# Optimization experiments

Hardware: AMD Instinct MI355X
Metric: run time of the kernel (lower is better)

The kernel has to match this reference:

```python
import jax, jax.numpy as jnp
import numpy as np

N = 10000   # function nodes
E = 160000  # edges (avg in/out degree ~16)
C = 8       # hidden channels per function node (fix_hidden_channels=True)
B = 64      # batch
EPS = 1e-5


def setup_inputs() -> dict:
    key = jax.random.key(0)
    ks = jax.random.split(key, 6)
    x = jax.random.normal(ks[0], (B, E), jnp.float32)
    # xavier-ish scale for fan_in ~ avg_degree=16
    w1 = jax.random.normal(ks[1], (E, C), jnp.float32) * 0.25
    b1 = jnp.zeros((N, C), jnp.float32)
    w3 = jax.random.normal(ks[2], (E, C), jnp.float32) * 0.25
    b3 = jnp.zeros((E,), jnp.float32)
    gamma = jnp.ones((N, C), jnp.float32)
    beta = jnp.zeros((N, C), jnp.float32)
    edge_src = jax.random.randint(ks[3], (E,), 0, N, dtype=jnp.int32)
    edge_dst = jax.random.randint(ks[4], (E,), 0, N, dtype=jnp.int32)
    return dict(x=x, w1=w1, b1=b1, gamma=gamma, beta=beta, w3=w3, b3=b3,
                edge_src=edge_src, edge_dst=edge_dst)


def reference(x, w1, b1, gamma, beta, w3, b3, edge_src, edge_dst):
    # --- lin1: SparseLinear (E -> N*C); W1[e, (v,k)] != 0 iff v == dst(e) ---
    # out1[b, v, k] = sum_{e: dst(e)==v} x[b, e] * w1[e, k] + b1[v, k]
    vals = x.T[:, :, None] * w1[:, None, :]                    # [E, B, C]
    h = jax.ops.segment_sum(vals, edge_dst, num_segments=N)    # [N, B, C]
    h = jnp.transpose(h, (1, 0, 2)) + b1                       # [B, N, C]
    # --- GroupLayerNorm: normalize over each node's C-channel group ---
    mu = jnp.mean(h, axis=-1, keepdims=True)
    var = jnp.var(h, axis=-1, keepdims=True)
    h = (h - mu) * jax.lax.rsqrt(var + EPS) * gamma + beta
    # --- nonlin (ELU); dropout p=0 in eval mode -> identity ---
    h = jax.nn.elu(h)
    # --- lin3: SparseLinear (N*C -> E); W3[(v,k), e] != 0 iff v == src(e) ---
    # out[b, e] = sum_k h[b, src(e), k] * w3[e, k] + b3[e]
    g = h[:, edge_src, :]                                      # [B, E, C]
    out = jnp.einsum('bec,ec->be', g, w3) + b3                 # [B, E]
    # --- residual ---
    return out + x
```

## Files before the change

### kernel.cpp

```cpp
#include <hip/hip_runtime.h>

#define N_NODES 10000
#define N_EDGES 160000
#define NC 8
#define PAD 64
#define LN_EPS 1e-5f

typedef _Float16 h4_t __attribute__((ext_vector_type(4)));
typedef _Float16 h8_t __attribute__((ext_vector_type(8)));

__device__ __forceinline__ int swz(int e, int b) {
  return e * 64 + ((((b >> 2) ^ ((e >> 2) & 15)) << 2) | (b & 3));
}

__global__ void __launch_bounds__(256) prep_kernel(
    const float* __restrict__ x, const int* __restrict__ edst,
    const float* __restrict__ w1, int* __restrict__ cur_dst,
    _Float16* __restrict__ xT_d, _Float16* __restrict__ w1_h) {
  __shared__ float tile[64 * 64];
  __shared__ int pP[64];
  const int e0 = blockIdx.x * 64;
  const int t = threadIdx.x;

  if (t < 64) {
    const int e = e0 + t;
    const int n = edst[e];
    int r = atomicAdd(&cur_dst[n], 1);
    if (r >= PAD) r = PAD - 1;
    const int p = (n << 6) + r;
    pP[t] = p;
    const float4* wp1 = (const float4*)(w1 + (size_t)e * NC);
    const float4 wa = wp1[0], wb = wp1[1];
    h8_t hw;
    hw[0] = (_Float16)wa.x; hw[1] = (_Float16)wa.y;
    hw[2] = (_Float16)wa.z; hw[3] = (_Float16)wa.w;
    hw[4] = (_Float16)wb.x; hw[5] = (_Float16)wb.y;
    hw[6] = (_Float16)wb.z; hw[7] = (_Float16)wb.w;
    *(h8_t*)&w1_h[(size_t)p * NC] = hw;
  }

  const int u = t & 15;
  const int row = t >> 4;
#pragma unroll
  for (int j = 0; j < 4; ++j) {
    const int b = j * 16 + row;
    const float4 xv = *(const float4*)&x[(size_t)b * N_EDGES + e0 + 4 * u];
    tile[swz(4 * u + 0, b)] = xv.x;
    tile[swz(4 * u + 1, b)] = xv.y;
    tile[swz(4 * u + 2, b)] = xv.z;
    tile[swz(4 * u + 3, b)] = xv.w;
  }
  __syncthreads();
#pragma unroll
  for (int j = 0; j < 4; ++j) {
    const int r = j * 16 + row;
    const float4 vv = *(const float4*)&tile[r * 64 + ((u ^ ((r >> 2) & 15)) << 2)];
    h4_t hv;
    hv[0] = (_Float16)vv.x; hv[1] = (_Float16)vv.y;
    hv[2] = (_Float16)vv.z; hv[3] = (_Float16)vv.w;
    *(h4_t*)&xT_d[(size_t)pP[r] * 64 + 4 * u] = hv;
  }
}

__global__ void __launch_bounds__(256) node_kernel(
    const _Float16* __restrict__ xT_d, const _Float16* __restrict__ w1_h,
    const float* __restrict__ b1, const float* __restrict__ gamma,
    const float* __restrict__ beta, const int* __restrict__ cur_dst,
    _Float16* __restrict__ v) {
  const int n = blockIdx.x * 4 + (threadIdx.x >> 6);
  const int b = threadIdx.x & 63;

  float a[NC];
#pragma unroll
  for (int c = 0; c < NC; ++c) a[c] = 0.f;

  const int s0 = n << 6;
  const int s1 = s0 + cur_dst[n];
  int i = s0;
  for (; i + 4 <= s1; i += 4) {
    float xe[4];
#pragma unroll
    for (int k = 0; k < 4; ++k) xe[k] = (float)xT_d[(size_t)(i + k) * 64 + b];
    h8_t wl[4];
#pragma unroll
    for (int k = 0; k < 4; ++k) wl[k] = *(const h8_t*)&w1_h[(size_t)(i + k) * NC];
#pragma unroll
    for (int k = 0; k < 4; ++k) {
#pragma unroll
      for (int c = 0; c < NC; ++c) a[c] += xe[k] * (float)wl[k][c];
    }
  }
  for (; i < s1; ++i) {
    const float xe = (float)xT_d[(size_t)i * 64 + b];
    const h8_t wl = *(const h8_t*)&w1_h[(size_t)i * NC];
#pragma unroll
    for (int c = 0; c < NC; ++c) a[c] += xe * (float)wl[c];
  }

  const float4* b1p = (const float4*)(b1 + (size_t)n * NC);
  const float4 b1a = b1p[0], b1b = b1p[1];
  a[0] += b1a.x; a[1] += b1a.y; a[2] += b1a.z; a[3] += b1a.w;
  a[4] += b1b.x; a[5] += b1b.y; a[6] += b1b.z; a[7] += b1b.w;

  float mu = 0.f;
#pragma unroll
  for (int c = 0; c < NC; ++c) mu += a[c];
  mu *= 0.125f;
  float var = 0.f;
#pragma unroll
  for (int c = 0; c < NC; ++c) { a[c] -= mu; var += a[c] * a[c]; }
  var *= 0.125f;
  const float rs = rsqrtf(var + LN_EPS);

  const float4* gp = (const float4*)(gamma + (size_t)n * NC);
  const float4 ga = gp[0], gb = gp[1];
  const float4* bp = (const float4*)(beta + (size_t)n * NC);
  const float4 ba = bp[0], bb = bp[1];
  float w[NC];
  w[0] = a[0] * rs * ga.x + ba.x;  w[1] = a[1] * rs * ga.y + ba.y;
  w[2] = a[2] * rs * ga.z + ba.z;  w[3] = a[3] * rs * ga.w + ba.w;
  w[4] = a[4] * rs * gb.x + bb.x;  w[5] = a[5] * rs * gb.y + bb.y;
  w[6] = a[6] * rs * gb.z + bb.z;  w[7] = a[7] * rs * gb.w + bb.w;
#pragma unroll
  for (int c = 0; c < NC; ++c) w[c] = w[c] > 0.f ? w[c] : expm1f(w[c]);

  h8_t hv;
#pragma unroll
  for (int c = 0; c < NC; ++c) hv[c] = (_Float16)w[c];
  *(h8_t*)&v[(size_t)n * 512 + b * NC] = hv;
}

__global__ void __launch_bounds__(256) edge_kernel(
    const _Float16* __restrict__ v, const float* __restrict__ w3,
    const float* __restrict__ b3, const float* __restrict__ x,
    const int* __restrict__ esrc, float* __restrict__ out) {
  __shared__ float tile[64 * 64];
  const int e0 = blockIdx.x * 64;
  const int t = threadIdx.x;
  const int w = t >> 6;
  const int b = t & 63;
  const int u = t & 15;
  const int row = t >> 4;

  int sidx = 0;
  if (b < 16) sidx = esrc[e0 + w * 16 + b];

  h8_t hv[16];
#pragma unroll
  for (int r = 0; r < 16; ++r) {
    const int s = __shfl(sidx, r, 64);
    hv[r] = *(const h8_t*)&v[(size_t)s * 512 + b * NC];
  }
  const float4 bb = *(const float4*)&b3[e0 + 4 * u];
  float4 xb[4];
#pragma unroll
  for (int j = 0; j < 4; ++j) {
    const int bo = j * 16 + row;
    xb[j] = *(const float4*)&x[(size_t)bo * N_EDGES + e0 + 4 * u];
  }

#pragma unroll
  for (int r = 0; r < 16; ++r) {
    const float4* wp = (const float4*)(w3 + (size_t)(e0 + w * 16 + r) * NC);
    const float4 wa = wp[0], wb = wp[1];
    const float dot =
        (float)hv[r][0] * wa.x + (float)hv[r][1] * wa.y +
        (float)hv[r][2] * wa.z + (float)hv[r][3] * wa.w +
        (float)hv[r][4] * wb.x + (float)hv[r][5] * wb.y +
        (float)hv[r][6] * wb.z + (float)hv[r][7] * wb.w;
    tile[swz(w * 16 + r, b)] = dot;
  }
  __syncthreads();

#pragma unroll
  for (int j = 0; j < 4; ++j) {
    const int bo = j * 16 + row;
    const float o0 = tile[swz(4 * u + 0, bo)];
    const float o1 = tile[swz(4 * u + 1, bo)];
    const float o2 = tile[swz(4 * u + 2, bo)];
    const float o3 = tile[swz(4 * u + 3, bo)];
    float4 o;
    o.x = o0 + bb.x + xb[j].x;  o.y = o1 + bb.y + xb[j].y;
    o.z = o2 + bb.z + xb[j].z;  o.w = o3 + bb.w + xb[j].w;
    *(float4*)&out[(size_t)bo * N_EDGES + e0 + 4 * u] = o;
  }
}

extern "C" void kernel_launch(void* const* d_in, const int* in_sizes, int n_in,
                              void* d_out, int out_size, void* d_ws, size_t ws_size,
                              hipStream_t stream) {
  const float* x     = (const float*)d_in[0];
  const float* w1    = (const float*)d_in[1];
  const float* b1    = (const float*)d_in[2];
  const float* gamma = (const float*)d_in[3];
  const float* beta  = (const float*)d_in[4];
  const float* w3    = (const float*)d_in[5];
  const float* b3    = (const float*)d_in[6];
  const int* esrc    = (const int*)d_in[7];
  const int* edst    = (const int*)d_in[8];
  float* out = (float*)d_out;

  char* ws = (char*)d_ws;
  size_t off = 0;
  auto alloc = [&](size_t bytes) -> void* {
    void* p = ws + off;
    off += (bytes + 255) & ~(size_t)255;
    return p;
  };
  _Float16* xT_d = (_Float16*)alloc((size_t)N_NODES * PAD * 64 * 2);
  _Float16* w1_h = (_Float16*)alloc((size_t)N_NODES * PAD * NC * 2);
  _Float16* v    = (_Float16*)alloc((size_t)N_NODES * 512 * 2);
  int* cur_dst   = (int*)alloc((size_t)N_NODES * 4);

  hipMemsetAsync(cur_dst, 0, (size_t)N_NODES * 4, stream);

  prep_kernel<<<N_EDGES / 64, 256, 0, stream>>>(x, edst, w1, cur_dst, xT_d, w1_h);
  node_kernel<<<N_NODES / 4, 256, 0, stream>>>(xT_d, w1_h, b1, gamma, beta,
                                               cur_dst, v);
  edge_kernel<<<N_EDGES / 64, 256, 0, stream>>>(v, w3, b3, x, esrc, out);
}
```

Before: 165.9 us.

## Fuse three kernels and memset into one cooperative persistent kernel with grid syncs

Replaces the memset plus prep, node and edge kernels with a single cooperative kernel. Blocks loop over tiles in grid-stride fashion and are separated by grid.sync barriers, with the grid sized from occupancy. This removes launch gaps between stages, in exchange for grid-wide barrier cost, the loss of __launch_bounds__ (which may raise register pressure), and extra __syncthreads in the looped tiles.

```diff
diff --git a/kernel.cpp b/kernel.cpp
--- a/kernel.cpp
+++ b/kernel.cpp
@@ -1,4 +1,7 @@
 #include <hip/hip_runtime.h>
+#include <hip/hip_cooperative_groups.h>
+
+namespace cg = cooperative_groups;
 
 #define N_NODES 10000
 #define N_EDGES 160000
@@ -13,176 +16,189 @@
   return e * 64 + ((((b >> 2) ^ ((e >> 2) & 15)) << 2) | (b & 3));
 }
 
-__global__ void __launch_bounds__(256) prep_kernel(
-    const float* __restrict__ x, const int* __restrict__ edst,
-    const float* __restrict__ w1, int* __restrict__ cur_dst,
-    _Float16* __restrict__ xT_d, _Float16* __restrict__ w1_h) {
+__global__ void fused_kernel(
+    const float* __restrict__ x, const float* __restrict__ w1,
+    const float* __restrict__ b1, const float* __restrict__ gamma,
+    const float* __restrict__ beta, const float* __restrict__ w3,
+    const float* __restrict__ b3, const int* __restrict__ esrc,
+    const int* __restrict__ edst, float* __restrict__ out,
+    _Float16* __restrict__ xT_d, _Float16* __restrict__ w1_h,
+    _Float16* __restrict__ v, int* __restrict__ cur_dst) {
+  cg::grid_group grid = cg::this_grid();
   __shared__ float tile[64 * 64];
   __shared__ int pP[64];
-  const int e0 = blockIdx.x * 64;
   const int t = threadIdx.x;
-
-  if (t < 64) {
-    const int e = e0 + t;
-    const int n = edst[e];
-    int r = atomicAdd(&cur_dst[n], 1);
-    if (r >= PAD) r = PAD - 1;
-    const int p = (n << 6) + r;
-    pP[t] = p;
-    const float4* wp1 = (const float4*)(w1 + (size_t)e * NC);
-    const float4 wa = wp1[0], wb = wp1[1];
-    h8_t hw;
-    hw[0] = (_Float16)wa.x; hw[1] = (_Float16)wa.y;
-    hw[2] = (_Float16)wa.z; hw[3] = (_Float16)wa.w;
-    hw[4] = (_Float16)wb.x; hw[5] = (_Float16)wb.y;
-    hw[6] = (_Float16)wb.z; hw[7] = (_Float16)wb.w;
-    *(h8_t*)&w1_h[(size_t)p * NC] = hw;
-  }
-
-  const int u = t & 15;
-  const int row = t >> 4;
-#pragma unroll
-  for (int j = 0; j < 4; ++j) {
-    const int b = j * 16 + row;
-    const float4 xv = *(const float4*)&x[(size_t)b * N_EDGES + e0 + 4 * u];
-    tile[swz(4 * u + 0, b)] = xv.x;
-    tile[swz(4 * u + 1, b)] = xv.y;
-    tile[swz(4 * u + 2, b)] = xv.z;
-    tile[swz(4 * u + 3, b)] = xv.w;
-  }
-  __syncthreads();
-#pragma unroll
-  for (int j = 0; j < 4; ++j) {
-    const int r = j * 16 + row;
-    const float4 vv = *(const float4*)&tile[r * 64 + ((u ^ ((r >> 2) & 15)) << 2)];
-    h4_t hv;
-    hv[0] = (_Float16)vv.x; hv[1] = (_Float16)vv.y;
-    hv[2] = (_Float16)vv.z; hv[3] = (_Float16)vv.w;
-    *(h4_t*)&xT_d[(size_t)pP[r] * 64 + 4 * u] = hv;
-  }
-}
-
-__global__ void __launch_bounds__(256) node_kernel(
-    const _Float16* __restrict__ xT_d, const _Float16* __restrict__ w1_h,
-    const float* __restrict__ b1, const float* __restrict__ gamma,
-    const float* __restrict__ beta, const int* __restrict__ cur_dst,
-    _Float16* __restrict__ v) {
-  const int n = blockIdx.x * 4 + (threadIdx.x >> 6);
-  const int b = threadIdx.x & 63;
-
-  float a[NC];
-#pragma unroll
-  for (int c = 0; c < NC; ++c) a[c] = 0.f;
-
-  const int s0 = n << 6;
-  const int s1 = s0 + cur_dst[n];
-  int i = s0;
-  for (; i + 4 <= s1; i += 4) {
-    float xe[4];
-#pragma unroll
-    for (int k = 0; k < 4; ++k) xe[k] = (float)xT_d[(size_t)(i + k) * 64 + b];
-    h8_t wl[4];
-#pragma unroll
-    for (int k = 0; k < 4; ++k) wl[k] = *(const h8_t*)&w1_h[(size_t)(i + k) * NC];
-#pragma unroll
-    for (int k = 0; k < 4; ++k) {
-#pragma unroll
-      for (int c = 0; c < NC; ++c) a[c] += xe[k] * (float)wl[k][c];
+  const int nb = gridDim.x;
+
+  for (int i = blockIdx.x * 256 + t; i < N_NODES; i += nb * 256) cur_dst[i] = 0;
+  grid.sync();
+
+  {
+    const int u = t & 15;
+    const int row = t >> 4;
+    for (int tl = blockIdx.x; tl < N_EDGES / 64; tl += nb) {
+      const int e0 = tl * 64;
+      if (t < 64) {
+        const int e = e0 + t;
+        const int n = edst[e];
+        int r = atomicAdd(&cur_dst[n], 1);
+        if (r >= PAD) r = PAD - 1;
+        const int p = (n << 6) + r;
+        pP[t] = p;
+        const float4* wp1 = (const float4*)(w1 + (size_t)e * NC);
+        const float4 wa = wp1[0], wb = wp1[1];
+        h8_t hw;
+        hw[0] = (_Float16)wa.x; hw[1] = (_Float16)wa.y;
+        hw[2] = (_Float16)wa.z; hw[3] = (_Float16)wa.w;
+        hw[4] = (_Float16)wb.x; hw[5] = (_Float16)wb.y;
+        hw[6] = (_Float16)wb.z; hw[7] = (_Float16)wb.w;
+        *(h8_t*)&w1_h[(size_t)p * NC] = hw;
+      }
+#pragma unroll
+      for (int j = 0; j < 4; ++j) {
+        const int b = j * 16 + row;
+        const float4 xv = *(const float4*)&x[(size_t)b * N_EDGES + e0 + 4 * u];
+        tile[swz(4 * u + 0, b)] = xv.x;
+        tile[swz(4 * u + 1, b)] = xv.y;
+        tile[swz(4 * u + 2, b)] = xv.z;
+        tile[swz(4 * u + 3, b)] = xv.w;
+      }
+      __syncthreads();
+#pragma unroll
+      for (int j = 0; j < 4; ++j) {
+        const int r = j * 16 + row;
+        const float4 vv =
+            *(const float4*)&tile[r * 64 + ((u ^ ((r >> 2) & 15)) << 2)];
+        h4_t hv;
+        hv[0] = (_Float16)vv.x; hv[1] = (_Float16)vv.y;
+        hv[2] = (_Float16)vv.z; hv[3] = (_Float16)vv.w;
+        *(h4_t*)&xT_d[(size_t)pP[r] * 64 + 4 * u] = hv;
+      }
+      __syncthreads();
     }
   }
-  for (; i < s1; ++i) {
-    const float xe = (float)xT_d[(size_t)i * 64 + b];
-    const h8_t wl = *(const h8_t*)&w1_h[(size_t)i * NC];
-#pragma unroll
-    for (int c = 0; c < NC; ++c) a[c] += xe * (float)wl[c];
-  }
-
-  const float4* b1p = (const float4*)(b1 + (size_t)n * NC);
-  const float4 b1a = b1p[0], b1b = b1p[1];
-  a[0] += b1a.x; a[1] += b1a.y; a[2] += b1a.z; a[3] += b1a.w;
-  a[4] += b1b.x; a[5] += b1b.y; a[6] += b1b.z; a[7] += b1b.w;
-
-  float mu = 0.f;
-#pragma unroll
-  for (int c = 0; c < NC; ++c) mu += a[c];
-  mu *= 0.125f;
-  float var = 0.f;
-#pragma unroll
-  for (int c = 0; c < NC; ++c) { a[c] -= mu; var += a[c] * a[c]; }
-  var *= 0.125f;
-  const float rs = rsqrtf(var + LN_EPS);
-
-  const float4* gp = (const float4*)(gamma + (size_t)n * NC);
-  const float4 ga = gp[0], gb = gp[1];
-  const float4* bp = (const float4*)(beta + (size_t)n * NC);
-  const float4 ba = bp[0], bb = bp[1];
-  float w[NC];
-  w[0] = a[0] * rs * ga.x + ba.x;  w[1] = a[1] * rs * ga.y + ba.y;
-  w[2] = a[2] * rs * ga.z + ba.z;  w[3] = a[3] * rs * ga.w + ba.w;
-  w[4] = a[4] * rs * gb.x + bb.x;  w[5] = a[5] * rs * gb.y + bb.y;
-  w[6] = a[6] * rs * gb.z + bb.z;  w[7] = a[7] * rs * gb.w + bb.w;
-#pragma unroll
-  for (int c = 0; c < NC; ++c) w[c] = w[c] > 0.f ? w[c] : expm1f(w[c]);
-
-  h8_t hv;
-#pragma unroll
-  for (int c = 0; c < NC; ++c) hv[c] = (_Float16)w[c];
-  *(h8_t*)&v[(size_t)n * 512 + b * NC] = hv;
-}
-
-__global__ void __launch_bounds__(256) edge_kernel(
-    const _Float16* __restrict__ v, const float* __restrict__ w3,
-    const float* __restrict__ b3, const float* __restrict__ x,
-    const int* __restrict__ esrc, float* __restrict__ out) {
-  __shared__ float tile[64 * 64];
-  const int e0 = blockIdx.x * 64;
-  const int t = threadIdx.x;
-  const int w = t >> 6;
-  const int b = t & 63;
-  const int u = t & 15;
-  const int row = t >> 4;
-
-  int sidx = 0;
-  if (b < 16) sidx = esrc[e0 + w * 16 + b];
-
-  h8_t hv[16];
-#pragma unroll
-  for (int r = 0; r < 16; ++r) {
-    const int s = __shfl(sidx, r, 64);
-    hv[r] = *(const h8_t*)&v[(size_t)s * 512 + b * NC];
-  }
-  const float4 bb = *(const float4*)&b3[e0 + 4 * u];
-  float4 xb[4];
-#pragma unroll
-  for (int j = 0; j < 4; ++j) {
-    const int bo = j * 16 + row;
-    xb[j] = *(const float4*)&x[(size_t)bo * N_EDGES + e0 + 4 * u];
-  }
-
-#pragma unroll
-  for (int r = 0; r < 16; ++r) {
-    const float4* wp = (const float4*)(w3 + (size_t)(e0 + w * 16 + r) * NC);
-    const float4 wa = wp[0], wb = wp[1];
-    const float dot =
-        (float)hv[r][0] * wa.x + (float)hv[r][1] * wa.y +
-        (float)hv[r][2] * wa.z + (float)hv[r][3] * wa.w +
-        (float)hv[r][4] * wb.x + (float)hv[r][5] * wb.y +
-        (float)hv[r][6] * wb.z + (float)hv[r][7] * wb.w;
-    tile[swz(w * 16 + r, b)] = dot;
-  }
-  __syncthreads();
-
-#pragma unroll
-  for (int j = 0; j < 4; ++j) {
-    const int bo = j * 16 + row;
-    const float o0 = tile[swz(4 * u + 0, bo)];
-    const float o1 = tile[swz(4 * u + 1, bo)];
-    const float o2 = tile[swz(4 * u + 2, bo)];
-    const float o3 = tile[swz(4 * u + 3, bo)];
-    float4 o;
-    o.x = o0 + bb.x + xb[j].x;  o.y = o1 + bb.y + xb[j].y;
-    o.z = o2 + bb.z + xb[j].z;  o.w = o3 + bb.w + xb[j].w;
-    *(float4*)&out[(size_t)bo * N_EDGES + e0 + 4 * u] = o;
+  grid.sync();
+
+  {
+    const int wid = t >> 6;
+    const int b = t & 63;
+    for (int g = blockIdx.x; g < N_NODES / 4; g += nb) {
+      const int n = g * 4 + wid;
+
+      float a[NC];
+#pragma unroll
+      for (int c = 0; c < NC; ++c) a[c] = 0.f;
+
+      const int s0 = n << 6;
+      const int s1 = s0 + cur_dst[n];
+      int i = s0;
+      for (; i + 4 <= s1; i += 4) {
+        float xe[4];
+#pragma unroll
+        for (int k = 0; k < 4; ++k) xe[k] = (float)xT_d[(size_t)(i + k) * 64 + b];
+        h8_t wl[4];
+#pragma unroll
+        for (int k = 0; k < 4; ++k) wl[k] = *(const h8_t*)&w1_h[(size_t)(i + k) * NC];
+#pragma unroll
+        for (int k = 0; k < 4; ++k) {
+#pragma unroll
+          for (int c = 0; c < NC; ++c) a[c] += xe[k] * (float)wl[k][c];
+        }
+      }
+      for (; i < s1; ++i) {
+        const float xe = (float)xT_d[(size_t)i * 64 + b];
+        const h8_t wl = *(const h8_t*)&w1_h[(size_t)i * NC];
+#pragma unroll
+        for (int c = 0; c < NC; ++c) a[c] += xe * (float)wl[c];
+      }
+
+      const float4* b1p = (const float4*)(b1 + (size_t)n * NC);
+      const float4 b1a = b1p[0], b1b = b1p[1];
+      a[0] += b1a.x; a[1] += b1a.y; a[2] += b1a.z; a[3] += b1a.w;
+      a[4] += b1b.x; a[5] += b1b.y; a[6] += b1b.z; a[7] += b1b.w;
+
+      float mu = 0.f;
+#pragma unroll
+      for (int c = 0; c < NC; ++c) mu += a[c];
+      mu *= 0.125f;
+      float var = 0.f;
+#pragma unroll
+      for (int c = 0; c < NC; ++c) { a[c] -= mu; var += a[c] * a[c]; }
+      var *= 0.125f;
+      const float rs = rsqrtf(var + LN_EPS);
+
+      const float4* gp = (const float4*)(gamma + (size_t)n * NC);
+      const float4 ga = gp[0], gb = gp[1];
+      const float4* bp = (const float4*)(beta + (size_t)n * NC);
+      const float4 ba = bp[0], bb = bp[1];
+      float w[NC];
+      w[0] = a[0] * rs * ga.x + ba.x;  w[1] = a[1] * rs * ga.y + ba.y;
+      w[2] = a[2] * rs * ga.z + ba.z;  w[3] = a[3] * rs * ga.w + ba.w;
+      w[4] = a[4] * rs * gb.x + bb.x;  w[5] = a[5] * rs * gb.y + bb.y;
+      w[6] = a[6] * rs * gb.z + bb.z;  w[7] = a[7] * rs * gb.w + bb.w;
+#pragma unroll
+      for (int c = 0; c < NC; ++c) w[c] = w[c] > 0.f ? w[c] : expm1f(w[c]);
+
+      h8_t hv;
+#pragma unroll
+      for (int c = 0; c < NC; ++c) hv[c] = (_Float16)w[c];
+      *(h8_t*)&v[(size_t)n * 512 + b * NC] = hv;
+    }
+  }
+  grid.sync();
+
+  {
+    const int w = t >> 6;
+    const int b = t & 63;
+    const int u = t & 15;
+    const int row = t >> 4;
+    for (int tl = blockIdx.x; tl < N_EDGES / 64; tl += nb) {
+      const int e0 = tl * 64;
+
+      int sidx = 0;
+      if (b < 16) sidx = esrc[e0 + w * 16 + b];
+
+      h8_t hv[16];
+#pragma unroll
+      for (int r = 0; r < 16; ++r) {
+        const int s = __shfl(sidx, r, 64);
+        hv[r] = *(const h8_t*)&v[(size_t)s * 512 + b * NC];
+      }
+      const float4 bb = *(const float4*)&b3[e0 + 4 * u];
+      float4 xb[4];
+#pragma unroll
+      for (int j = 0; j < 4; ++j) {
+        const int bo = j * 16 + row;
+        xb[j] = *(const float4*)&x[(size_t)bo * N_EDGES + e0 + 4 * u];
+      }
+
+#pragma unroll
+      for (int r = 0; r < 16; ++r) {
+        const float4* wp = (const float4*)(w3 + (size_t)(e0 + w * 16 + r) * NC);
+        const float4 wa = wp[0], wb = wp[1];
+        const float dot =
+            (float)hv[r][0] * wa.x + (float)hv[r][1] * wa.y +
+            (float)hv[r][2] * wa.z + (float)hv[r][3] * wa.w +
+            (float)hv[r][4] * wb.x + (float)hv[r][5] * wb.y +
+            (float)hv[r][6] * wb.z + (float)hv[r][7] * wb.w;
+        tile[swz(w * 16 + r, b)] = dot;
+      }
+      __syncthreads();
+
+#pragma unroll
+      for (int j = 0; j < 4; ++j) {
+        const int bo = j * 16 + row;
+        const float o0 = tile[swz(4 * u + 0, bo)];
+        const float o1 = tile[swz(4 * u + 1, bo)];
+        const float o2 = tile[swz(4 * u + 2, bo)];
+        const float o3 = tile[swz(4 * u + 3, bo)];
+        float4 o;
+        o.x = o0 + bb.x + xb[j].x;  o.y = o1 + bb.y + xb[j].y;
+        o.z = o2 + bb.z + xb[j].z;  o.w = o3 + bb.w + xb[j].w;
+        *(float4*)&out[(size_t)bo * N_EDGES + e0 + 4 * u] = o;
+      }
+      __syncthreads();
+    }
   }
 }
 
@@ -212,10 +228,20 @@
   _Float16* v    = (_Float16*)alloc((size_t)N_NODES * 512 * 2);
   int* cur_dst   = (int*)alloc((size_t)N_NODES * 4);
 
-  hipMemsetAsync(cur_dst, 0, (size_t)N_NODES * 4, stream);
-
-  prep_kernel<<<N_EDGES / 64, 256, 0, stream>>>(x, edst, w1, cur_dst, xT_d, w1_h);
-  node_kernel<<<N_NODES / 4, 256, 0, stream>>>(xT_d, w1_h, b1, gamma, beta,
-                                               cur_dst, v);
-  edge_kernel<<<N_EDGES / 64, 256, 0, stream>>>(v, w3, b3, x, esrc, out);
+  static int grid_blocks = 0;
+  if (grid_blocks == 0) {
+    int bpc = 0;
+    if (hipOccupancyMaxActiveBlocksPerMultiprocessor(&bpc, fused_kernel, 256, 0)
+            != hipSuccess || bpc < 1)
+      bpc = 2;
+    grid_blocks = bpc * 256;
+    if (grid_blocks > 2500) grid_blocks = 2500;
+  }
+
+  void* kargs[] = {(void*)&x,    (void*)&w1,   (void*)&b1,  (void*)&gamma,
+                   (void*)&beta, (void*)&w3,   (void*)&b3,  (void*)&esrc,
+                   (void*)&edst, (void*)&out,  (void*)&xT_d, (void*)&w1_h,
+                   (void*)&v,    (void*)&cur_dst};
+  hipLaunchCooperativeKernel((const void*)fused_kernel, dim3(grid_blocks),
+                             dim3(256), kargs, 0, stream);
 }
```

After: 402.7 us. 2.43x slower.

## Store edge index lists instead of scattering transposed x and w1 by destination

Applied to the files above, without the earlier changes.

The prep kernel no longer scatters the transposed x rows and the fp16 w1 rows into per-destination padded slots. It writes x transposed in edge order plus a per-node list of edge ids, and the node kernel gathers through that list, reading w1 directly in fp32. This turns the scattered writes in prep into coalesced ones and shrinks the padded workspace. In exchange the node kernel does an extra dependent index load and random gathers, with w1 now read at full precision. Overflow beyond PAD edges per node now drops those edges, where before they overwrote the last slot.

```diff
diff --git a/kernel.cpp b/kernel.cpp
--- a/kernel.cpp
+++ b/kernel.cpp
@@ -13,30 +13,19 @@
   return e * 64 + ((((b >> 2) ^ ((e >> 2) & 15)) << 2) | (b & 3));
 }
 
-__global__ void __launch_bounds__(256) prep_kernel(
+__global__ void __launch_bounds__(256) transpose_kernel(
     const float* __restrict__ x, const int* __restrict__ edst,
-    const float* __restrict__ w1, int* __restrict__ cur_dst,
-    _Float16* __restrict__ xT_d, _Float16* __restrict__ w1_h) {
+    int* __restrict__ cur_dst, _Float16* __restrict__ xT,
+    int* __restrict__ ein) {
   __shared__ float tile[64 * 64];
-  __shared__ int pP[64];
   const int e0 = blockIdx.x * 64;
   const int t = threadIdx.x;
 
   if (t < 64) {
     const int e = e0 + t;
     const int n = edst[e];
-    int r = atomicAdd(&cur_dst[n], 1);
-    if (r >= PAD) r = PAD - 1;
-    const int p = (n << 6) + r;
-    pP[t] = p;
-    const float4* wp1 = (const float4*)(w1 + (size_t)e * NC);
-    const float4 wa = wp1[0], wb = wp1[1];
-    h8_t hw;
-    hw[0] = (_Float16)wa.x; hw[1] = (_Float16)wa.y;
-    hw[2] = (_Float16)wa.z; hw[3] = (_Float16)wa.w;
-    hw[4] = (_Float16)wb.x; hw[5] = (_Float16)wb.y;
-    hw[6] = (_Float16)wb.z; hw[7] = (_Float16)wb.w;
-    *(h8_t*)&w1_h[(size_t)p * NC] = hw;
+    const int r = atomicAdd(&cur_dst[n], 1);
+    if (r < PAD) ein[(n << 6) + r] = e;
   }
 
   const int u = t & 15;
@@ -58,15 +47,15 @@
     h4_t hv;
     hv[0] = (_Float16)vv.x; hv[1] = (_Float16)vv.y;
     hv[2] = (_Float16)vv.z; hv[3] = (_Float16)vv.w;
-    *(h4_t*)&xT_d[(size_t)pP[r] * 64 + 4 * u] = hv;
+    *(h4_t*)&xT[(size_t)(e0 + r) * 64 + 4 * u] = hv;
   }
 }
 
 __global__ void __launch_bounds__(256) node_kernel(
-    const _Float16* __restrict__ xT_d, const _Float16* __restrict__ w1_h,
-    const float* __restrict__ b1, const float* __restrict__ gamma,
-    const float* __restrict__ beta, const int* __restrict__ cur_dst,
-    _Float16* __restrict__ v) {
+    const _Float16* __restrict__ xT, const int* __restrict__ ein,
+    const float* __restrict__ w1, const float* __restrict__ b1,
+    const float* __restrict__ gamma, const float* __restrict__ beta,
+    const int* __restrict__ cur_dst, _Float16* __restrict__ v) {
   const int n = blockIdx.x * 4 + (threadIdx.x >> 6);
   const int b = threadIdx.x & 63;
 
@@ -75,26 +64,39 @@
   for (int c = 0; c < NC; ++c) a[c] = 0.f;
 
   const int s0 = n << 6;
-  const int s1 = s0 + cur_dst[n];
+  const int deg = min(cur_dst[n], PAD);
+  const int s1 = s0 + deg;
   int i = s0;
   for (; i + 4 <= s1; i += 4) {
+    int e[4];
+#pragma unroll
+    for (int k = 0; k < 4; ++k) e[k] = ein[i + k];
     float xe[4];
 #pragma unroll
-    for (int k = 0; k < 4; ++k) xe[k] = (float)xT_d[(size_t)(i + k) * 64 + b];
-    h8_t wl[4];
-#pragma unroll
-    for (int k = 0; k < 4; ++k) wl[k] = *(const h8_t*)&w1_h[(size_t)(i + k) * NC];
+    for (int k = 0; k < 4; ++k) xe[k] = (float)xT[(size_t)e[k] * 64 + b];
+    float4 wa[4], wb[4];
 #pragma unroll
     for (int k = 0; k < 4; ++k) {
-#pragma unroll
-      for (int c = 0; c < NC; ++c) a[c] += xe[k] * (float)wl[k][c];
+      const float4* wp = (const float4*)(w1 + (size_t)e[k] * NC);
+      wa[k] = wp[0]; wb[k] = wp[1];
     }
+#pragma unroll
+    for (int k = 0; k < 4; ++k) {
+      a[0] += xe[k] * wa[k].x;  a[1] += xe[k] * wa[k].y;
+      a[2] += xe[k] * wa[k].z;  a[3] += xe[k] * wa[k].w;
+      a[4] += xe[k] * wb[k].x;  a[5] += xe[k] * wb[k].y;
+      a[6] += xe[k] * wb[k].z;  a[7] += xe[k] * wb[k].w;
+    }
   }
   for (; i < s1; ++i) {
-    const float xe = (float)xT_d[(size_t)i * 64 + b];
-    const h8_t wl = *(const h8_t*)&w1_h[(size_t)i * NC];
-#pragma unroll
-    for (int c = 0; c < NC; ++c) a[c] += xe * (float)wl[c];
+    const int e = ein[i];
+    const float xe = (float)xT[(size_t)e * 64 + b];
+    const float4* wp = (const float4*)(w1 + (size_t)e * NC);
+    const float4 wa = wp[0], wb = wp[1];
+    a[0] += xe * wa.x;  a[1] += xe * wa.y;
+    a[2] += xe * wa.z;  a[3] += xe * wa.w;
+    a[4] += xe * wb.x;  a[5] += xe * wb.y;
+    a[6] += xe * wb.z;  a[7] += xe * wb.w;
   }
 
   const float4* b1p = (const float4*)(b1 + (size_t)n * NC);
@@ -207,15 +209,15 @@
     off += (bytes + 255) & ~(size_t)255;
     return p;
   };
-  _Float16* xT_d = (_Float16*)alloc((size_t)N_NODES * PAD * 64 * 2);
-  _Float16* w1_h = (_Float16*)alloc((size_t)N_NODES * PAD * NC * 2);
-  _Float16* v    = (_Float16*)alloc((size_t)N_NODES * 512 * 2);
-  int* cur_dst   = (int*)alloc((size_t)N_NODES * 4);
+  _Float16* xT  = (_Float16*)alloc((size_t)N_EDGES * 64 * 2);
+  int* ein      = (int*)alloc((size_t)N_NODES * PAD * 4);
+  _Float16* v   = (_Float16*)alloc((size_t)N_NODES * 512 * 2);
+  int* cur_dst  = (int*)alloc((size_t)N_NODES * 4);
 
   hipMemsetAsync(cur_dst, 0, (size_t)N_NODES * 4, stream);
 
-  prep_kernel<<<N_EDGES / 64, 256, 0, stream>>>(x, edst, w1, cur_dst, xT_d, w1_h);
-  node_kernel<<<N_NODES / 4, 256, 0, stream>>>(xT_d, w1_h, b1, gamma, beta,
+  transpose_kernel<<<N_EDGES / 64, 256, 0, stream>>>(x, edst, cur_dst, xT, ein);
+  node_kernel<<<N_NODES / 4, 256, 0, stream>>>(xT, ein, w1, b1, gamma, beta,
                                                cur_dst, v);
   edge_kernel<<<N_EDGES / 64, 256, 0, stream>>>(v, w3, b3, x, esrc, out);
 }
```

After: 169.3 us. 2.1% more time.

## Process 256 edges per block in prep and edge kernels

Applied to the files above, without the earlier changes.

Both the prep and edge kernels now handle 256 edges per block instead of 64. The prep kernel stages x in a padded fp16 shared tile, so the transpose and precision conversion happen together. The edge kernel loops over four 64-edge sub-tiles, holds all outputs in registers and writes them at the end. This cuts block count to 625, meant to lower per-block overhead and give wider contiguous row segments. The cost is more registers per thread and fewer blocks to spread across CUs, which may hurt latency hiding.

```diff
diff --git a/kernel.cpp b/kernel.cpp
--- a/kernel.cpp
+++ b/kernel.cpp
@@ -17,12 +17,12 @@
     const float* __restrict__ x, const int* __restrict__ edst,
     const float* __restrict__ w1, int* __restrict__ cur_dst,
     _Float16* __restrict__ xT_d, _Float16* __restrict__ w1_h) {
-  __shared__ float tile[64 * 64];
-  __shared__ int pP[64];
-  const int e0 = blockIdx.x * 64;
+  __shared__ _Float16 tile[256 * 72];
+  __shared__ int pP[256];
+  const int e0 = blockIdx.x * 256;
   const int t = threadIdx.x;
 
-  if (t < 64) {
+  {
     const int e = e0 + t;
     const int n = edst[e];
     int r = atomicAdd(&cur_dst[n], 1);
@@ -42,23 +42,25 @@
   const int u = t & 15;
   const int row = t >> 4;
 #pragma unroll
-  for (int j = 0; j < 4; ++j) {
-    const int b = j * 16 + row;
-    const float4 xv = *(const float4*)&x[(size_t)b * N_EDGES + e0 + 4 * u];
-    tile[swz(4 * u + 0, b)] = xv.x;
-    tile[swz(4 * u + 1, b)] = xv.y;
-    tile[swz(4 * u + 2, b)] = xv.z;
-    tile[swz(4 * u + 3, b)] = xv.w;
+  for (int s = 0; s < 4; ++s) {
+#pragma unroll
+    for (int j = 0; j < 4; ++j) {
+      const int b = j * 16 + row;
+      const float4 xv =
+          *(const float4*)&x[(size_t)b * N_EDGES + e0 + 64 * s + 4 * u];
+      const int el = 64 * s + 4 * u;
+      tile[(el + 0) * 72 + b] = (_Float16)xv.x;
+      tile[(el + 1) * 72 + b] = (_Float16)xv.y;
+      tile[(el + 2) * 72 + b] = (_Float16)xv.z;
+      tile[(el + 3) * 72 + b] = (_Float16)xv.w;
+    }
   }
   __syncthreads();
 #pragma unroll
-  for (int j = 0; j < 4; ++j) {
-    const int r = j * 16 + row;
-    const float4 vv = *(const float4*)&tile[r * 64 + ((u ^ ((r >> 2) & 15)) << 2)];
-    h4_t hv;
-    hv[0] = (_Float16)vv.x; hv[1] = (_Float16)vv.y;
-    hv[2] = (_Float16)vv.z; hv[3] = (_Float16)vv.w;
-    *(h4_t*)&xT_d[(size_t)pP[r] * 64 + 4 * u] = hv;
+  for (int m = 0; m < 16; ++m) {
+    const int rr = m * 16 + row;
+    const h4_t hv = *(const h4_t*)&tile[rr * 72 + 4 * u];
+    *(h4_t*)&xT_d[(size_t)pP[rr] * 64 + 4 * u] = hv;
   }
 }
 
@@ -135,54 +137,68 @@
     const float* __restrict__ b3, const float* __restrict__ x,
     const int* __restrict__ esrc, float* __restrict__ out) {
   __shared__ float tile[64 * 64];
-  const int e0 = blockIdx.x * 64;
+  const int e0 = blockIdx.x * 256;
   const int t = threadIdx.x;
   const int w = t >> 6;
   const int b = t & 63;
   const int u = t & 15;
   const int row = t >> 4;
 
-  int sidx = 0;
-  if (b < 16) sidx = esrc[e0 + w * 16 + b];
-
-  h8_t hv[16];
-#pragma unroll
-  for (int r = 0; r < 16; ++r) {
-    const int s = __shfl(sidx, r, 64);
-    hv[r] = *(const h8_t*)&v[(size_t)s * 512 + b * NC];
-  }
-  const float4 bb = *(const float4*)&b3[e0 + 4 * u];
-  float4 xb[4];
+  float4 bb[4];
+#pragma unroll
+  for (int p = 0; p < 4; ++p)
+    bb[p] = *(const float4*)&b3[e0 + p * 64 + 4 * u];
+
+  float4 ob[4][4];
+#pragma unroll
+  for (int p = 0; p < 4; ++p) {
+    const int ep = e0 + p * 64;
+    int sidx = 0;
+    if (b < 16) sidx = esrc[ep + w * 16 + b];
+
+    h8_t hv[16];
+#pragma unroll
+    for (int r = 0; r < 16; ++r) {
+      const int s = __shfl(sidx, r, 64);
+      hv[r] = *(const h8_t*)&v[(size_t)s * 512 + b * NC];
+    }
+
+#pragma unroll
+    for (int r = 0; r < 16; ++r) {
+      const float4* wp = (const float4*)(w3 + (size_t)(ep + w * 16 + r) * NC);
+      const float4 wa = wp[0], wb = wp[1];
+      const float dot =
+          (float)hv[r][0] * wa.x + (float)hv[r][1] * wa.y +
+          (float)hv[r][2] * wa.z + (float)hv[r][3] * wa.w +
+          (float)hv[r][4] * wb.x + (float)hv[r][5] * wb.y +
+          (float)hv[r][6] * wb.z + (float)hv[r][7] * wb.w;
+      tile[swz(w * 16 + r, b)] = dot;
+    }
+    __syncthreads();
+
+#pragma unroll
+    for (int j = 0; j < 4; ++j) {
+      const int bo = j * 16 + row;
+      const float o0 = tile[swz(4 * u + 0, bo)];
+      const float o1 = tile[swz(4 * u + 1, bo)];
+      const float o2 = tile[swz(4 * u + 2, bo)];
+      const float o3 = tile[swz(4 * u + 3, bo)];
+      const float4 xb = *(const float4*)&x[(size_t)bo * N_EDGES + ep + 4 * u];
+      float4 o;
+      o.x = o0 + bb[p].x + xb.x;  o.y = o1 + bb[p].y + xb.y;
+      o.z = o2 + bb[p].z + xb.z;  o.w = o3 + bb[p].w + xb.w;
+      ob[p][j] = o;
+    }
+    __syncthreads();
+  }
+
 #pragma unroll
   for (int j = 0; j < 4; ++j) {
     const int bo = j * 16 + row;
-    xb[j] = *(const float4*)&x[(size_t)bo * N_EDGES + e0 + 4 * u];
-  }
-
-#pragma unroll
-  for (int r = 0; r < 16; ++r) {
-    const float4* wp = (const float4*)(w3 + (size_t)(e0 + w * 16 + r) * NC);
-    const float4 wa = wp[0], wb = wp[1];
-    const float dot =
-        (float)hv[r][0] * wa.x + (float)hv[r][1] * wa.y +
-        (float)hv[r][2] * wa.z + (float)hv[r][3] * wa.w +
-        (float)hv[r][4] * wb.x + (float)hv[r][5] * wb.y +
-        (float)hv[r][6] * wb.z + (float)hv[r][7] * wb.w;
-    tile[swz(w * 16 + r, b)] = dot;
-  }
-  __syncthreads();
-
-#pragma unroll
-  for (int j = 0; j < 4; ++j) {
-    const int bo = j * 16 + row;
-    const float o0 = tile[swz(4 * u + 0, bo)];
-    const float o1 = tile[swz(4 * u + 1, bo)];
-    const float o2 = tile[swz(4 * u + 2, bo)];
-    const float o3 = tile[swz(4 * u + 3, bo)];
-    float4 o;
-    o.x = o0 + bb.x + xb[j].x;  o.y = o1 + bb.y + xb[j].y;
-    o.z = o2 + bb.z + xb[j].z;  o.w = o3 + bb.w + xb[j].w;
-    *(float4*)&out[(size_t)bo * N_EDGES + e0 + 4 * u] = o;
+#pragma unroll
+    for (int p = 0; p < 4; ++p) {
+      *(float4*)&out[(size_t)bo * N_EDGES + e0 + p * 64 + 4 * u] = ob[p][j];
+    }
   }
 }
 
@@ -214,8 +230,8 @@
 
   hipMemsetAsync(cur_dst, 0, (size_t)N_NODES * 4, stream);
 
-  prep_kernel<<<N_EDGES / 64, 256, 0, stream>>>(x, edst, w1, cur_dst, xT_d, w1_h);
+  prep_kernel<<<N_EDGES / 256, 256, 0, stream>>>(x, edst, w1, cur_dst, xT_d, w1_h);
   node_kernel<<<N_NODES / 4, 256, 0, stream>>>(xT_d, w1_h, b1, gamma, beta,
                                                cur_dst, v);
-  edge_kernel<<<N_EDGES / 64, 256, 0, stream>>>(v, w3, b3, x, esrc, out);
-}
+  edge_kernel<<<N_EDGES / 256, 256, 0, stream>>>(v, w3, b3, x, esrc, out);
+}
```

Result: slower. 176.7 us (+6.5%).
